# Optimization experiments

Hardware: AMD Instinct MI355X
Metric: run time of the kernel (lower is better)

The kernel has to match this reference:

```python
import jax, jax.numpy as jnp
import numpy as np

B, S, D = 2, 2048, 2048
RANK = 512
N_HEADS = 16
DROPOUT_RATE = 0.1
KEEP = 1.0 - DROPOUT_RATE  # original safe_dropout scales by 1/keep even when deterministic


def setup_inputs() -> dict:
    key = jax.random.key(0)
    ks = jax.random.split(key, 9)
    return {
        "x": jax.random.normal(ks[0], (B, S, D), jnp.float32),
        "g_Q": jax.random.uniform(ks[1], (B, S, RANK), jnp.float32),
        "g_K": jax.random.uniform(ks[2], (B, S, RANK), jnp.float32),
        "g_V": jax.random.uniform(ks[3], (B, S, RANK), jnp.float32),
        "qk_read": jax.random.normal(ks[4], (RANK, D), jnp.float32) * 0.02,
        "qk_write": jax.random.normal(ks[5], (RANK, D), jnp.float32) * 0.02,
        "v_read": jax.random.normal(ks[6], (RANK, D), jnp.float32) * 0.02,
        "v_write": jax.random.normal(ks[7], (RANK, D), jnp.float32) * 0.02,
        "W_O": jax.random.normal(ks[8], (D, D), jnp.float32) * 0.02,
    }


def _gated_lowrank(x, g, rd, wr):
    # g * (x @ rd.T) @ wr : [B,S,D] -> [B,S,rank] -> [B,S,D]
    return (g * jnp.einsum('bsd,rd->bsr', x, rd)) @ wr


def reference(x, g_Q, g_K, g_V, qk_read, qk_write, v_read, v_write, W_O):
    Bx, Sx, Dx = x.shape
    d_head = Dx // N_HEADS

    Q = _gated_lowrank(x, g_Q, qk_read, qk_write)
    K = _gated_lowrank(x, g_K, qk_read, qk_write)
    V = _gated_lowrank(x, g_V, v_read, v_write)

    Q = Q.reshape(Bx, Sx, N_HEADS, d_head).transpose(0, 2, 1, 3)
    K = K.reshape(Bx, Sx, N_HEADS, d_head).transpose(0, 2, 1, 3)
    V = V.reshape(Bx, Sx, N_HEADS, d_head).transpose(0, 2, 1, 3)

    scale = jnp.sqrt(jnp.float32(d_head))
    scores = jnp.einsum('bhsd,bhtd->bhst', Q, K) / scale  # [B,H,S,S]
    causal = jnp.tril(jnp.ones((Sx, Sx), dtype=jnp.bool_))
    scores = jnp.where(causal, scores, jnp.finfo(scores.dtype).min)
    attn_w = jax.nn.softmax(scores, axis=-1)
    attn_w = attn_w / KEEP  # deterministic branch of original safe_dropout

    out = jnp.einsum('bhst,bhtd->bhsd', attn_w, V)
    out = out.transpose(0, 2, 1, 3).reshape(Bx, Sx, Dx)
    out = out @ W_O
    out = out / KEEP  # deterministic dropout scaling
    return out
```

## Files before the change

kernel.cpp:

```cpp
#include <hip/hip_runtime.h>
#include <cstdint>
#include <cstddef>

typedef unsigned short u16;
typedef unsigned int u32;
typedef __attribute__((ext_vector_type(4))) float f32x4;
typedef __attribute__((ext_vector_type(8))) __bf16 bf16x8;
typedef __attribute__((ext_vector_type(8))) u16 u16x8;
typedef __attribute__((ext_vector_type(4))) u16 u16x4;

__device__ __forceinline__ u16 f2bf(float x) {
  u32 u = __builtin_bit_cast(u32, x);
  u += 0x7fffu + ((u >> 16) & 1u);
  return (u16)(u >> 16);
}
__device__ __forceinline__ float bf2f(u16 b) {
  return __builtin_bit_cast(float, (u32)b << 16);
}
__device__ __forceinline__ bf16x8 ldfrag(const u16* p) {
  return __builtin_bit_cast(bf16x8, *(const u16x8*)p);
}
__device__ __forceinline__ void gload_lds16(const void* g, void* l) {
  auto gp = (const __attribute__((address_space(1))) u32*)g;
  auto lp = (__attribute__((address_space(3))) u32*)l;
  __builtin_amdgcn_global_load_lds(gp, lp, 16, 0, 0);
}
#define MFMA16(a, b, c) __builtin_amdgcn_mfma_f32_16x16x32_bf16(a, b, c, 0, 0, 0)


__global__ void cvt_kernel(const float* __restrict__ in, u16* __restrict__ out, int n) {
  int i = (blockIdx.x * blockDim.x + threadIdx.x) * 4;
  if (i >= n) return;
  f32x4 v = *(const f32x4*)(in + i);
  u16x4 r = { f2bf(v[0]), f2bf(v[1]), f2bf(v[2]), f2bf(v[3]) };
  *(u16x4*)(out + i) = r;
}

__global__ void tcvt_kernel(const float* __restrict__ in, u16* __restrict__ out, int R, int C) {
  __shared__ float tile[32][33];
  int bx = blockIdx.x * 32, by = blockIdx.y * 32;
  int tx = threadIdx.x, ty = threadIdx.y;
#pragma unroll
  for (int i = 0; i < 32; i += 8)
    tile[ty + i][tx] = in[(size_t)(by + ty + i) * C + bx + tx];
  __syncthreads();
#pragma unroll
  for (int i = 0; i < 32; i += 8)
    out[(size_t)(bx + ty + i) * R + by + tx] = f2bf(tile[tx][ty + i]);
}

__global__ void gate_kernel(const float* __restrict__ gq, const float* __restrict__ gk,
                            const float* __restrict__ gv, const u16* __restrict__ Pcat,
                            u16* __restrict__ Aq, u16* __restrict__ Ak, u16* __restrict__ Av,
                            int n) {
  int i = (blockIdx.x * blockDim.x + threadIdx.x) * 4;
  if (i >= n) return;
  int s = i >> 9;
  int r = i & 511;
  u16x4 pq = *(const u16x4*)(Pcat + (size_t)s * 1024 + r);
  u16x4 pv = *(const u16x4*)(Pcat + (size_t)s * 1024 + 512 + r);
  f32x4 q = *(const f32x4*)(gq + i);
  f32x4 k = *(const f32x4*)(gk + i);
  f32x4 v = *(const f32x4*)(gv + i);
  u16x4 aq, ak, av;
#pragma unroll
  for (int j = 0; j < 4; ++j) {
    float pf = bf2f(pq[j]);
    float vf = bf2f(pv[j]);
    aq[j] = f2bf(q[j] * pf);
    ak[j] = f2bf(k[j] * pf);
    av[j] = f2bf(v[j] * vf);
  }
  *(u16x4*)(Aq + i) = aq;
  *(u16x4*)(Ak + i) = ak;
  *(u16x4*)(Av + i) = av;
}

template <bool F32OUT>
__global__ void gemm_bt(const u16* __restrict__ A, const u16* __restrict__ Bt,
                        void* __restrict__ Cp, int M, int N, int K, float scale) {
  __shared__ u16 Al[128 * 32];
  __shared__ u16 Bl[128 * 32];
  const int tid = threadIdx.x;
  const int lane = tid & 63;
  const int w = tid >> 6;
  const int wr = (w >> 1) * 64;
  const int wc = (w & 1) * 64;
  const size_t bm = (size_t)blockIdx.y * 128;
  const size_t bn = (size_t)blockIdx.x * 128;

  f32x4 acc[4][4] = {};

  const int srow = lane >> 2;
  const int sch = lane & 3;
  const int kc = lane >> 4;
  const int rl = lane & 15;

  for (int kt = 0; kt < K; kt += 32) {
#pragma unroll
    for (int half = 0; half < 2; ++half) {
      int rb = half * 64 + w * 16;
      int row = rb + srow;
      int ch = sch ^ ((row >> 1) & 3);
      gload_lds16(A + (bm + row) * (size_t)K + kt + ch * 8, &Al[rb * 32]);
    }
#pragma unroll
    for (int half = 0; half < 2; ++half) {
      int rb = half * 64 + w * 16;
      int row = rb + srow;
      int ch = sch ^ ((row >> 1) & 3);
      gload_lds16(Bt + (bn + row) * (size_t)K + kt + ch * 8, &Bl[rb * 32]);
    }
    asm volatile("s_waitcnt vmcnt(0)" ::: "memory");
    __syncthreads();

    bf16x8 af[4], bfr[4];
#pragma unroll
    for (int m = 0; m < 4; ++m) {
      int row = wr + m * 16 + rl;
      af[m] = ldfrag(&Al[row * 32 + (kc ^ ((row >> 1) & 3)) * 8]);
    }
#pragma unroll
    for (int n = 0; n < 4; ++n) {
      int row = wc + n * 16 + rl;
      bfr[n] = ldfrag(&Bl[row * 32 + (kc ^ ((row >> 1) & 3)) * 8]);
    }
#pragma unroll
    for (int m = 0; m < 4; ++m)
#pragma unroll
      for (int n = 0; n < 4; ++n)
        acc[m][n] = MFMA16(af[m], bfr[n], acc[m][n]);
    __syncthreads();
  }

  const int r0 = (lane >> 4) * 4;
#pragma unroll
  for (int m = 0; m < 4; ++m) {
    size_t grow = bm + wr + m * 16 + r0;
#pragma unroll
    for (int n = 0; n < 4; ++n) {
      size_t gcol = bn + wc + n * 16 + rl;
#pragma unroll
      for (int r = 0; r < 4; ++r) {
        float v = acc[m][n][r] * scale;
        if constexpr (F32OUT)
          ((float*)Cp)[(grow + r) * (size_t)N + gcol] = v;
        else
          ((u16*)Cp)[(grow + r) * (size_t)N + gcol] = f2bf(v);
      }
    }
  }
}

__global__ __launch_bounds__(512, 1) void attn_kernel(const u16* __restrict__ Q,
                                                      const u16* __restrict__ Kg,
                                                      const u16* __restrict__ Vt,
                                                      u16* __restrict__ AO) {
  __shared__ u16 Kl[2][64 * 128];
  __shared__ u16 Vl[2][128 * 64];
  __shared__ u16 Pl[8][16 * 64];

  const int tid = threadIdx.x;
  const int lane = tid & 63;
  const int w = tid >> 6;
  const int pi = blockIdx.x;
  const int b = blockIdx.y >> 4;
  const int h = blockIdx.y & 15;

  const int rl = lane & 15;
  const int g4 = lane >> 4;

  u16* pl = &Pl[w][0];
  const float SC = 0.1275255128608411f;
  const float THR = 10.0f;

  bf16x8 ones;
  {
    u16x8 ou;
#pragma unroll
    for (int j = 0; j < 8; ++j) ou[j] = 0x3F80;
    ones = __builtin_bit_cast(bf16x8, ou);
  }

  auto stage = [&](int buf, int t0) {
    {
      int roff = lane >> 4;
      int cch = lane & 15;
#pragma unroll
      for (int i = 0; i < 2; ++i) {
        int rb = w * 8 + i * 4;
        int row = rb + roff;
        int ch = cch ^ (row & 7);
        gload_lds16(Kg + ((size_t)b * 2048 + t0 + row) * 2048 + h * 128 + ch * 8,
                    &Kl[buf][rb * 128]);
      }
    }
    {
      int roff = lane >> 3;
      int cch = lane & 7;
#pragma unroll
      for (int i = 0; i < 2; ++i) {
        int rb = w * 16 + i * 8;
        int row = rb + roff;
        int ch = cch ^ (row & 7);
        gload_lds16(Vt + (size_t)(h * 128 + row) * 4096 + (size_t)b * 2048 + t0 + ch * 8,
                    &Vl[buf][rb * 64]);
      }
    }
  };

  const int qbs[2] = {pi, 15 - pi};

  stage(0, 0);
  __syncthreads();
  int cur = 0;

#pragma unroll 1
  for (int ph = 0; ph < 2; ++ph) {
    const int qb = qbs[ph];
    const int ntiles = 2 * qb + 2;
    const int qbase = qb * 128 + w * 16;
    const int wmax = qbase + 15;
    const size_t qrow0 = (size_t)b * 2048 + (size_t)qb * 128;

    bf16x8 qf[4];
    {
      const u16* qp = Q + (qrow0 + w * 16 + rl) * 2048 + h * 128 + g4 * 8;
#pragma unroll
      for (int ks = 0; ks < 4; ++ks) qf[ks] = ldfrag(qp + ks * 32);
    }

    float m_r[4], l_r[4];
#pragma unroll
    for (int r = 0; r < 4; ++r) { m_r[r] = -3.0e38f; l_r[r] = 0.f; }
    f32x4 oacc[8] = {};

#pragma unroll 1
    for (int t = 0; t < ntiles; ++t) {
      const int t0 = t * 64;
      if (t + 1 < ntiles) stage(cur ^ 1, (t + 1) * 64);
      else if (ph == 0) stage(cur ^ 1, 0);

      if (t0 <= wmax) {
        float p[4][4];
        float pmax[4] = {-3.0e38f, -3.0e38f, -3.0e38f, -3.0e38f};
        __builtin_amdgcn_s_setprio(1);
#pragma unroll
        for (int nf = 0; nf < 4; ++nf) {
          f32x4 c = {};
          int trow = nf * 16 + rl;
#pragma unroll
          for (int ks = 0; ks < 4; ++ks) {
            bf16x8 kf = ldfrag(&Kl[cur][trow * 128 + ((ks * 4 + g4) ^ (trow & 7)) * 8]);
            c = MFMA16(qf[ks], kf, c);
          }
          int tc = t0 + nf * 16 + rl;
          int fragq = qbase + g4 * 4;
          if (t0 + 63 > qbase) {
#pragma unroll
            for (int r = 0; r < 4; ++r)
              p[nf][r] = (tc <= fragq + r) ? c[r] * SC : -3.0e38f;
          } else {
#pragma unroll
            for (int r = 0; r < 4; ++r) p[nf][r] = c[r] * SC;
          }
#pragma unroll
          for (int r = 0; r < 4; ++r) pmax[r] = fmaxf(pmax[r], p[nf][r]);
        }
        __builtin_amdgcn_s_setprio(0);

#pragma unroll
        for (int off = 1; off < 16; off <<= 1)
#pragma unroll
          for (int r = 0; r < 4; ++r)
            pmax[r] = fmaxf(pmax[r], __shfl_xor(pmax[r], off, 16));

        float mg = -3.0e38f;
#pragma unroll
        for (int r = 0; r < 4; ++r) mg = fmaxf(mg, pmax[r] - m_r[r]);
        if (__any(mg > THR)) {
#pragma unroll
          for (int r = 0; r < 4; ++r) {
            float mn = fmaxf(m_r[r], pmax[r]);
            float alpha = exp2f(m_r[r] - mn);
            m_r[r] = mn;
            l_r[r] *= alpha;
#pragma unroll
            for (int nf = 0; nf < 8; ++nf) oacc[nf][r] *= alpha;
          }
        }

#pragma unroll
        for (int nf = 0; nf < 4; ++nf) {
          int tt = nf * 16 + rl;
#pragma unroll
          for (int r = 0; r < 4; ++r) {
            float e = exp2f(p[nf][r] - m_r[r]);
            int q = g4 * 4 + r;
            pl[q * 64 + ((tt >> 3) ^ (q & 7)) * 8 + (tt & 7)] = f2bf(e);
          }
        }

        __builtin_amdgcn_s_setprio(1);
        f32x4 rs = {};
#pragma unroll
        for (int ks = 0; ks < 2; ++ks) {
          bf16x8 pa = ldfrag(&pl[rl * 64 + ((ks * 4 + g4) ^ (rl & 7)) * 8]);
#pragma unroll
          for (int nf = 0; nf < 8; ++nf) {
            int drow = nf * 16 + rl;
            bf16x8 vf = ldfrag(&Vl[cur][drow * 64 + ((ks * 4 + g4) ^ (drow & 7)) * 8]);
            oacc[nf] = MFMA16(pa, vf, oacc[nf]);
          }
          rs = MFMA16(pa, ones, rs);
        }
        __builtin_amdgcn_s_setprio(0);
#pragma unroll
        for (int r = 0; r < 4; ++r) l_r[r] += rs[r];
      }

      __syncthreads();
      cur ^= 1;
    }

#pragma unroll
    for (int nf = 0; nf < 8; ++nf) {
      size_t dc = (size_t)h * 128 + nf * 16 + rl;
#pragma unroll
      for (int r = 0; r < 4; ++r) {
        float v = oacc[nf][r] / l_r[r];
        AO[(qrow0 + w * 16 + g4 * 4 + r) * 2048 + dc] = f2bf(v);
      }
    }
  }
}


extern "C" void kernel_launch(void* const* d_in, const int* in_sizes, int n_in,
                              void* d_out, int out_size, void* d_ws, size_t ws_size,
                              hipStream_t stream) {
  const float* x = (const float*)d_in[0];
  const float* gQ = (const float*)d_in[1];
  const float* gK = (const float*)d_in[2];
  const float* gV = (const float*)d_in[3];
  const float* qkr = (const float*)d_in[4];
  const float* qkw = (const float*)d_in[5];
  const float* vr = (const float*)d_in[6];
  const float* vw = (const float*)d_in[7];
  const float* wo = (const float*)d_in[8];
  float* out = (float*)d_out;

  u16* p = (u16*)d_ws;
  u16* x_bf = p;   p += 8388608;
  u16* qkr_b = p;  p += 1048576;
  u16* vr_b = p;   p += 1048576;
  u16* qkwT = p;   p += 1048576;
  u16* vwT = p;    p += 1048576;
  u16* woT = p;    p += 4194304;
  u16* Pcat = p;   p += 4194304;
  u16* Aq = p;     p += 2097152;
  u16* Ak = p;     p += 2097152;
  u16* Av = p;     p += 2097152;
  u16* Qb = p;     p += 8388608;
  u16* Kb = p;     p += 8388608;
  u16* Vt = x_bf;
  u16* AO = Qb;

  cvt_kernel<<<8192, 256, 0, stream>>>(x, x_bf, 8388608);
  cvt_kernel<<<1024, 256, 0, stream>>>(qkr, qkr_b, 1048576);
  cvt_kernel<<<1024, 256, 0, stream>>>(vr, vr_b, 1048576);
  tcvt_kernel<<<dim3(64, 16), dim3(32, 8), 0, stream>>>(qkw, qkwT, 512, 2048);
  tcvt_kernel<<<dim3(64, 16), dim3(32, 8), 0, stream>>>(vw, vwT, 512, 2048);
  tcvt_kernel<<<dim3(64, 64), dim3(32, 8), 0, stream>>>(wo, woT, 2048, 2048);

  gemm_bt<false><<<dim3(8, 32), 256, 0, stream>>>(x_bf, qkr_b, Pcat, 4096, 1024, 2048, 1.f);

  gate_kernel<<<2048, 256, 0, stream>>>(gQ, gK, gV, Pcat, Aq, Ak, Av, 2097152);

  gemm_bt<false><<<dim3(16, 64), 256, 0, stream>>>(Aq, qkwT, Qb, 8192, 2048, 512, 1.f);

  gemm_bt<false><<<dim3(32, 16), 256, 0, stream>>>(vwT, Av, Vt, 2048, 4096, 512, 1.f);

  attn_kernel<<<dim3(8, 32), 512, 0, stream>>>(Qb, Kb, Vt, AO);

  gemm_bt<true><<<dim3(16, 32), 256, 0, stream>>>(AO, woT, out, 4096, 2048, 2048,
                                                  1.2345679012345678f);
}
```

Before: 258.7 us.

## Shrink attention blocks to 64 query rows with single-buffered V and aliased P

The attention kernel now uses 256-thread blocks covering 64 query rows, launched as 512 blocks with up to 3 resident per CU instead of one 512-thread block per CU. V is single-buffered and loaded each tile, and the probability tile reuses the current K buffer once a barrier confirms the QK reads are done. That cuts LDS use so more blocks fit per CU. The causal pairing of query blocks and the grid order are reorganised to balance work. The trade-off is less overlap on V loads, since a manual vmcnt wait plus barrier now sits inside each tile iteration.

Result: no change. 261.1 us (+1.0%).

```diff
diff --git a/kernel.cpp b/kernel.cpp
--- a/kernel.cpp
+++ b/kernel.cpp
@@ -152,25 +152,24 @@
   }
 }
 
-__global__ __launch_bounds__(512, 1) void attn_kernel(const u16* __restrict__ Q,
+__global__ __launch_bounds__(256, 3) void attn_kernel(const u16* __restrict__ Q,
                                                       const u16* __restrict__ Kg,
                                                       const u16* __restrict__ Vt,
                                                       u16* __restrict__ AO) {
   __shared__ u16 Kl[2][64 * 128];
-  __shared__ u16 Vl[2][128 * 64];
-  __shared__ u16 Pl[8][16 * 64];
+  __shared__ u16 Vl[128 * 64];
 
   const int tid = threadIdx.x;
   const int lane = tid & 63;
   const int w = tid >> 6;
-  const int pi = blockIdx.x;
-  const int b = blockIdx.y >> 4;
-  const int h = blockIdx.y & 15;
+  const int bh = blockIdx.x;
+  const int pi = blockIdx.y;
+  const int b = bh >> 4;
+  const int h = bh & 15;
 
   const int rl = lane & 15;
   const int g4 = lane >> 4;
 
-  u16* pl = &Pl[w][0];
   const float SC = 0.1275255128608411f;
   const float THR = 10.0f;
 
@@ -182,46 +181,43 @@
     ones = __builtin_bit_cast(bf16x8, ou);
   }
 
-  auto stage = [&](int buf, int t0) {
-    {
-      int roff = lane >> 4;
-      int cch = lane & 15;
-#pragma unroll
-      for (int i = 0; i < 2; ++i) {
-        int rb = w * 8 + i * 4;
-        int row = rb + roff;
-        int ch = cch ^ (row & 7);
-        gload_lds16(Kg + ((size_t)b * 2048 + t0 + row) * 2048 + h * 128 + ch * 8,
-                    &Kl[buf][rb * 128]);
-      }
-    }
-    {
-      int roff = lane >> 3;
-      int cch = lane & 7;
-#pragma unroll
-      for (int i = 0; i < 2; ++i) {
-        int rb = w * 16 + i * 8;
-        int row = rb + roff;
-        int ch = cch ^ (row & 7);
-        gload_lds16(Vt + (size_t)(h * 128 + row) * 4096 + (size_t)b * 2048 + t0 + ch * 8,
-                    &Vl[buf][rb * 64]);
-      }
+  auto stageK = [&](int buf, int t0) {
+    int roff = lane >> 4;
+    int cch = lane & 15;
+#pragma unroll
+    for (int i = 0; i < 4; ++i) {
+      int rb = w * 16 + i * 4;
+      int row = rb + roff;
+      int ch = cch ^ (row & 7);
+      gload_lds16(Kg + ((size_t)b * 2048 + t0 + row) * 2048 + h * 128 + ch * 8,
+                  &Kl[buf][rb * 128]);
     }
   };
-
-  const int qbs[2] = {pi, 15 - pi};
-
-  stage(0, 0);
+  auto stageV = [&](int t0) {
+    int roff = lane >> 3;
+    int cch = lane & 7;
+#pragma unroll
+    for (int i = 0; i < 4; ++i) {
+      int rb = w * 32 + i * 8;
+      int row = rb + roff;
+      int ch = cch ^ (row & 7);
+      gload_lds16(Vt + (size_t)(h * 128 + row) * 4096 + (size_t)b * 2048 + t0 + ch * 8,
+                  &Vl[rb * 64]);
+    }
+  };
+
+  const int qbs[2] = {31 - pi, pi};
+
+  stageK(0, 0);
   __syncthreads();
   int cur = 0;
 
 #pragma unroll 1
   for (int ph = 0; ph < 2; ++ph) {
     const int qb = qbs[ph];
-    const int ntiles = 2 * qb + 2;
-    const int qbase = qb * 128 + w * 16;
-    const int wmax = qbase + 15;
-    const size_t qrow0 = (size_t)b * 2048 + (size_t)qb * 128;
+    const int ntiles = qb + 1;
+    const int qbase = qb * 64 + w * 16;
+    const size_t qrow0 = (size_t)b * 2048 + (size_t)qb * 64;
 
     bf16x8 qf[4];
     {
@@ -238,86 +234,94 @@
 #pragma unroll 1
     for (int t = 0; t < ntiles; ++t) {
       const int t0 = t * 64;
-      if (t + 1 < ntiles) stage(cur ^ 1, (t + 1) * 64);
-      else if (ph == 0) stage(cur ^ 1, 0);
-
-      if (t0 <= wmax) {
-        float p[4][4];
-        float pmax[4] = {-3.0e38f, -3.0e38f, -3.0e38f, -3.0e38f};
-        __builtin_amdgcn_s_setprio(1);
-#pragma unroll
-        for (int nf = 0; nf < 4; ++nf) {
-          f32x4 c = {};
-          int trow = nf * 16 + rl;
-#pragma unroll
-          for (int ks = 0; ks < 4; ++ks) {
-            bf16x8 kf = ldfrag(&Kl[cur][trow * 128 + ((ks * 4 + g4) ^ (trow & 7)) * 8]);
-            c = MFMA16(qf[ks], kf, c);
-          }
+      stageV(t0);
+      const bool pref = (t + 1 < ntiles) || (ph == 0);
+      if (pref) stageK(cur ^ 1, (t + 1 < ntiles) ? (t + 1) * 64 : 0);
+
+      float p[4][4];
+      float pmax[4] = {-3.0e38f, -3.0e38f, -3.0e38f, -3.0e38f};
+      __builtin_amdgcn_s_setprio(1);
+#pragma unroll
+      for (int nf = 0; nf < 4; ++nf) {
+        f32x4 c = {};
+        int trow = nf * 16 + rl;
+#pragma unroll
+        for (int ks = 0; ks < 4; ++ks) {
+          bf16x8 kf = ldfrag(&Kl[cur][trow * 128 + ((ks * 4 + g4) ^ (trow & 7)) * 8]);
+          c = MFMA16(qf[ks], kf, c);
+        }
+        if (t == qb) {
           int tc = t0 + nf * 16 + rl;
           int fragq = qbase + g4 * 4;
-          if (t0 + 63 > qbase) {
-#pragma unroll
-            for (int r = 0; r < 4; ++r)
-              p[nf][r] = (tc <= fragq + r) ? c[r] * SC : -3.0e38f;
-          } else {
-#pragma unroll
-            for (int r = 0; r < 4; ++r) p[nf][r] = c[r] * SC;
-          }
-#pragma unroll
-          for (int r = 0; r < 4; ++r) pmax[r] = fmaxf(pmax[r], p[nf][r]);
-        }
-        __builtin_amdgcn_s_setprio(0);
-
-#pragma unroll
-        for (int off = 1; off < 16; off <<= 1)
 #pragma unroll
           for (int r = 0; r < 4; ++r)
-            pmax[r] = fmaxf(pmax[r], __shfl_xor(pmax[r], off, 16));
-
-        float mg = -3.0e38f;
-#pragma unroll
-        for (int r = 0; r < 4; ++r) mg = fmaxf(mg, pmax[r] - m_r[r]);
-        if (__any(mg > THR)) {
-#pragma unroll
-          for (int r = 0; r < 4; ++r) {
-            float mn = fmaxf(m_r[r], pmax[r]);
-            float alpha = exp2f(m_r[r] - mn);
-            m_r[r] = mn;
-            l_r[r] *= alpha;
-#pragma unroll
-            for (int nf = 0; nf < 8; ++nf) oacc[nf][r] *= alpha;
-          }
-        }
-
-#pragma unroll
-        for (int nf = 0; nf < 4; ++nf) {
-          int tt = nf * 16 + rl;
-#pragma unroll
-          for (int r = 0; r < 4; ++r) {
-            float e = exp2f(p[nf][r] - m_r[r]);
-            int q = g4 * 4 + r;
-            pl[q * 64 + ((tt >> 3) ^ (q & 7)) * 8 + (tt & 7)] = f2bf(e);
-          }
-        }
-
-        __builtin_amdgcn_s_setprio(1);
-        f32x4 rs = {};
-#pragma unroll
-        for (int ks = 0; ks < 2; ++ks) {
-          bf16x8 pa = ldfrag(&pl[rl * 64 + ((ks * 4 + g4) ^ (rl & 7)) * 8]);
-#pragma unroll
-          for (int nf = 0; nf < 8; ++nf) {
-            int drow = nf * 16 + rl;
-            bf16x8 vf = ldfrag(&Vl[cur][drow * 64 + ((ks * 4 + g4) ^ (drow & 7)) * 8]);
-            oacc[nf] = MFMA16(pa, vf, oacc[nf]);
-          }
-          rs = MFMA16(pa, ones, rs);
-        }
-        __builtin_amdgcn_s_setprio(0);
-#pragma unroll
-        for (int r = 0; r < 4; ++r) l_r[r] += rs[r];
-      }
+            p[nf][r] = (tc <= fragq + r) ? c[r] * SC : -3.0e38f;
+        } else {
+#pragma unroll
+          for (int r = 0; r < 4; ++r) p[nf][r] = c[r] * SC;
+        }
+#pragma unroll
+        for (int r = 0; r < 4; ++r) pmax[r] = fmaxf(pmax[r], p[nf][r]);
+      }
+      __builtin_amdgcn_s_setprio(0);
+
+#pragma unroll
+      for (int off = 1; off < 16; off <<= 1)
+#pragma unroll
+        for (int r = 0; r < 4; ++r)
+          pmax[r] = fmaxf(pmax[r], __shfl_xor(pmax[r], off, 16));
+
+      float mg = -3.0e38f;
+#pragma unroll
+      for (int r = 0; r < 4; ++r) mg = fmaxf(mg, pmax[r] - m_r[r]);
+      if (__any(mg > THR)) {
+#pragma unroll
+        for (int r = 0; r < 4; ++r) {
+          float mn = fmaxf(m_r[r], pmax[r]);
+          float alpha = exp2f(m_r[r] - mn);
+          m_r[r] = mn;
+          l_r[r] *= alpha;
+#pragma unroll
+          for (int nf = 0; nf < 8; ++nf) oacc[nf][r] *= alpha;
+        }
+      }
+
+      float e[4][4];
+#pragma unroll
+      for (int nf = 0; nf < 4; ++nf)
+#pragma unroll
+        for (int r = 0; r < 4; ++r) e[nf][r] = exp2f(p[nf][r] - m_r[r]);
+
+      if (pref) asm volatile("s_waitcnt vmcnt(4)\n\ts_barrier" ::: "memory");
+      else      asm volatile("s_waitcnt vmcnt(0)\n\ts_barrier" ::: "memory");
+
+      u16* pl = &Kl[cur][w * 1024];
+#pragma unroll
+      for (int nf = 0; nf < 4; ++nf) {
+        int tt = nf * 16 + rl;
+#pragma unroll
+        for (int r = 0; r < 4; ++r) {
+          int q = g4 * 4 + r;
+          pl[q * 64 + ((tt >> 3) ^ (q & 7)) * 8 + (tt & 7)] = f2bf(e[nf][r]);
+        }
+      }
+
+      __builtin_amdgcn_s_setprio(1);
+      f32x4 rs = {};
+#pragma unroll
+      for (int ks = 0; ks < 2; ++ks) {
+        bf16x8 pa = ldfrag(&pl[rl * 64 + ((ks * 4 + g4) ^ (rl & 7)) * 8]);
+#pragma unroll
+        for (int nf = 0; nf < 8; ++nf) {
+          int drow = nf * 16 + rl;
+          bf16x8 vf = ldfrag(&Vl[drow * 64 + ((ks * 4 + g4) ^ (drow & 7)) * 8]);
+          oacc[nf] = MFMA16(pa, vf, oacc[nf]);
+        }
+        rs = MFMA16(pa, ones, rs);
+      }
+      __builtin_amdgcn_s_setprio(0);
+#pragma unroll
+      for (int r = 0; r < 4; ++r) l_r[r] += rs[r];
 
       __syncthreads();
       cur ^= 1;
@@ -381,7 +385,7 @@
 
   gemm_bt<false><<<dim3(32, 16), 256, 0, stream>>>(vwT, Av, Vt, 2048, 4096, 512, 1.f);
 
-  attn_kernel<<<dim3(8, 32), 512, 0, stream>>>(Qb, Kb, Vt, AO);
+  attn_kernel<<<dim3(32, 16), 256, 0, stream>>>(Qb, Kb, Vt, AO);
 
   gemm_bt<true><<<dim3(16, 32), 256, 0, stream>>>(AO, woT, out, 4096, 2048, 2048,
                                                   1.2345679012345678f);
```
